# Kernel optimization log

Measured on AMD Instinct MI355X. Metric: run time of the kernel, lower is better.

## Reference

```python
import jax, jax.numpy as jnp
import numpy as np

D = 256; NH = 8; HD = D // NH; L = 4; P = 4; NQ = 900; BS = 8; DFFN = 1024
SHAPES = np.array([[128, 128], [64, 64], [32, 32], [16, 16]])  # (H, W) per level, static metadata
NV = int((SHAPES[:, 0] * SHAPES[:, 1]).sum())
EPS = 1e-6


def setup_inputs():
    key = jax.random.key(0)
    ks = iter(jax.random.split(key, 48))

    def nrm(shape, scale=0.02):
        return jax.random.normal(next(ks), shape, jnp.float32) * scale

    lsi = np.concatenate([[0], np.cumsum(SHAPES[:, 0] * SHAPES[:, 1])[:-1]]).astype(np.int64)
    return {
        'tgt': nrm((NQ, BS, D), 1.0),
        'tgt_query_pos': nrm((NQ, BS, D), 1.0),
        'tgt_reference_points': jax.random.uniform(next(ks), (NQ, BS, L, 2), jnp.float32),
        'memory': nrm((NV, BS, D), 1.0),
        'memory_spatial_shapes': jnp.asarray(SHAPES, jnp.int32),
        'memory_level_start_index': jnp.asarray(lsi, jnp.int32),
        'w_norm_sa': jnp.ones((D,), jnp.float32),
        'w_norm_ca': jnp.ones((D,), jnp.float32),
        'w_norm_ffn': jnp.ones((D,), jnp.float32),
        'ls_sa': jnp.full((D,), 1e-4, jnp.float32),
        'ls_ca': jnp.full((D,), 1e-4, jnp.float32),
        'ls_ffn': jnp.full((D,), 1e-4, jnp.float32),
        'Wq': nrm((D, D)), 'Wk': nrm((D, D)), 'Wv': nrm((D, D)),
        'bq': jnp.zeros((D,), jnp.float32), 'bk': jnp.zeros((D,), jnp.float32), 'bv': jnp.zeros((D,), jnp.float32),
        'Wo_sa': nrm((D, D)), 'bo_sa': jnp.zeros((D,), jnp.float32),
        'Wv_proj': nrm((D, D)), 'bv_proj': jnp.zeros((D,), jnp.float32),
        'W_off': nrm((NH * L * P * 2, D)), 'b_off': nrm((NH * L * P * 2,), 0.1),
        'W_attn': nrm((NH * L * P, D)), 'b_attn': jnp.zeros((NH * L * P,), jnp.float32),
        'W_out_ca': nrm((D, D)), 'bo_ca': jnp.zeros((D,), jnp.float32),
        'Wg': nrm((DFFN, D)), 'bg': jnp.zeros((DFFN,), jnp.float32),
        'Wu': nrm((DFFN, D)), 'bu': jnp.zeros((DFFN,), jnp.float32),
        'Wf': nrm((D, DFFN)), 'bf': jnp.zeros((D,), jnp.float32),
    }


def rmsnorm(x, w):
    return x * jax.lax.rsqrt(jnp.mean(x * x, axis=-1, keepdims=True) + EPS) * w


def ms_deform_sample(v, loc, attw):
    # v: (bs, nv, NH, HD); loc: (bs, nq, NH, L, P, 2) normalized (x, y); attw: (bs, nq, NH, L, P)
    bs, nq = loc.shape[0], loc.shape[1]
    out = jnp.zeros((bs, nq, NH, HD), loc.dtype)
    b_idx = jnp.arange(bs)[:, None, None, None]
    h_idx = jnp.arange(NH)[None, None, :, None]
    start = 0
    for l in range(L):
        Hl, Wl = int(SHAPES[l, 0]), int(SHAPES[l, 1])
        vf = v[:, start:start + Hl * Wl]  # (bs, Hl*Wl, NH, HD)
        start += Hl * Wl
        # grid_sample(align_corners=False, padding=zeros) pixel mapping
        x = loc[:, :, :, l, :, 0] * Wl - 0.5
        y = loc[:, :, :, l, :, 1] * Hl - 0.5
        x0 = jnp.floor(x)
        y0 = jnp.floor(y)
        acc = jnp.zeros((bs, nq, NH, P, HD), loc.dtype)
        for dx in (0, 1):
            for dy in (0, 1):
                xi = x0 + dx
                yi = y0 + dy
                w = (1.0 - jnp.abs(x - xi)) * (1.0 - jnp.abs(y - yi))
                valid = (xi >= 0) & (xi <= Wl - 1) & (yi >= 0) & (yi <= Hl - 1)
                w = jnp.where(valid, w, 0.0)
                idx = (jnp.clip(yi, 0, Hl - 1) * Wl + jnp.clip(xi, 0, Wl - 1)).astype(jnp.int32)
                acc = acc + w[..., None] * vf[b_idx, idx, h_idx]  # (bs, nq, NH, P, HD)
        out = out + jnp.einsum('bqhp,bqhpd->bqhd', attw[:, :, :, l], acc)
    return out


def reference(tgt, tgt_query_pos, tgt_reference_points, memory, memory_spatial_shapes,
              memory_level_start_index, w_norm_sa, w_norm_ca, w_norm_ffn, ls_sa, ls_ca, ls_ffn,
              Wq, Wk, Wv, bq, bk, bv, Wo_sa, bo_sa, Wv_proj, bv_proj, W_off, b_off, W_attn,
              b_attn, W_out_ca, bo_ca, Wg, bg, Wu, bu, Wf, bf):
    nq, bs, d = tgt.shape
    # --- self-attention (pre-norm + LayerScale residual) ---
    xn = rmsnorm(tgt, w_norm_sa)
    qk = xn + tgt_query_pos
    q = (qk @ Wq.T + bq).reshape(nq, bs, NH, HD)
    k = (qk @ Wk.T + bk).reshape(nq, bs, NH, HD)
    vv = (xn @ Wv.T + bv).reshape(nq, bs, NH, HD)
    scores = jnp.einsum('qbhd,kbhd->bhqk', q, k) * (1.0 / np.sqrt(HD))
    attn = jax.nn.softmax(scores, axis=-1)
    sa = jnp.einsum('bhqk,kbhd->qbhd', attn, vv).reshape(nq, bs, d) @ Wo_sa.T + bo_sa
    tgt = tgt + ls_sa * sa
    # --- multi-scale deformable cross-attention (identity=zeros in original) ---
    xn = rmsnorm(tgt, w_norm_ca)
    qca = jnp.swapaxes(xn + tgt_query_pos, 0, 1)  # (bs, nq, d)
    val = (jnp.swapaxes(memory, 0, 1) @ Wv_proj.T + bv_proj).reshape(bs, -1, NH, HD)
    off = (qca @ W_off.T + b_off).reshape(bs, nq, NH, L, P, 2)
    attw = jax.nn.softmax((qca @ W_attn.T + b_attn).reshape(bs, nq, NH, L * P), axis=-1)
    attw = attw.reshape(bs, nq, NH, L, P)
    norm = jnp.asarray(SHAPES[:, ::-1].copy(), jnp.float32)  # (W, H) per level
    ref = jnp.swapaxes(tgt_reference_points, 0, 1)  # (bs, nq, L, 2)
    loc = ref[:, :, None, :, None, :] + off / norm[None, None, None, :, None, :]
    ca = ms_deform_sample(val, loc, attw).reshape(bs, nq, d) @ W_out_ca.T + bo_ca
    tgt = tgt + ls_ca * jnp.swapaxes(ca, 0, 1)
    # --- SwiGLU FFN ---
    xn = rmsnorm(tgt, w_norm_ffn)
    ffn = (jax.nn.silu(xn @ Wg.T + bg) * (xn @ Wu.T + bu)) @ Wf.T + bf
    return tgt + ls_ffn * ffn
```

## Files before the change

kernel.cpp:

```cpp
#include <hip/hip_runtime.h>

typedef unsigned short ushort_t;
typedef unsigned int uint32;
typedef __bf16 bf16x8 __attribute__((ext_vector_type(8)));
typedef float f32x4 __attribute__((ext_vector_type(4)));
typedef ushort_t us4 __attribute__((ext_vector_type(4)));

#define D_    256
#define NH_   8
#define HD_   32
#define NQ_   900
#define BS_   8
#define TOK_  7200
#define NV_   21760
#define QP_   928
#define DFFN_ 1024

__device__ __forceinline__ ushort_t f2bf(float x) {
    union { float f; uint32 u; } v; v.f = x;
    uint32 r = v.u + 0x7FFFu + ((v.u >> 16) & 1u);
    return (ushort_t)(r >> 16);
}
__device__ __forceinline__ float bf2f(ushort_t h) {
    union { uint32 u; float f; } v; v.u = ((uint32)h) << 16;
    return v.f;
}
__device__ __forceinline__ int imin(int a, int b) { return a < b ? a : b; }
__device__ __forceinline__ int imax(int a, int b) { return a > b ? a : b; }

__global__ __launch_bounds__(256) void cvtall_k(
    const float* __restrict__ s0, const float* __restrict__ s1, const float* __restrict__ s2,
    const float* __restrict__ s3, const float* __restrict__ s4, const float* __restrict__ s5,
    const float* __restrict__ s6, const float* __restrict__ s7, const float* __restrict__ s8,
    const float* __restrict__ s9, const float* __restrict__ s10, ushort_t* __restrict__ dst,
    const float* __restrict__ bq, const float* __restrict__ bk, const float* __restrict__ bv,
    const float* __restrict__ boff, const float* __restrict__ battn,
    float* __restrict__ bias_qkv, float* __restrict__ bias_ol) {
    int tid = threadIdx.x;
    if (blockIdx.x == 0) {
        bias_qkv[tid] = bq[tid];
        bias_qkv[256 + tid] = bk[tid];
        bias_qkv[512 + tid] = bv[tid];
        bias_ol[tid] = boff[tid];
        if (tid < 128) bias_ol[256 + tid] = battn[tid];
    }
    int id = blockIdx.x * 256 + tid;
    const float* s; int off;
    if      (id <  16384) { s = s0;  off = id; }
    else if (id <  32768) { s = s1;  off = id - 16384; }
    else if (id <  49152) { s = s2;  off = id - 32768; }
    else if (id <  65536) { s = s3;  off = id - 49152; }
    else if (id <  81920) { s = s4;  off = id - 65536; }
    else if (id <  98304) { s = s5;  off = id - 81920; }
    else if (id < 114688) { s = s6;  off = id - 98304; }
    else if (id < 122880) { s = s7;  off = id - 114688; }
    else if (id < 188416) { s = s8;  off = id - 122880; }
    else if (id < 253952) { s = s9;  off = id - 188416; }
    else                  { s = s10; off = id - 253952; }
    f32x4 v = *(const f32x4*)(s + (size_t)off * 4);
    us4 t;
#pragma unroll
    for (int e = 0; e < 4; e++) t[e] = f2bf(v[e]);
    *(us4*)(dst + (size_t)id * 4) = t;
}

__global__ __launch_bounds__(256) void rms_k(const float* __restrict__ x,
                                             const float* __restrict__ pos,
                                             const float* __restrict__ wn,
                                             ushort_t* __restrict__ xn_out,
                                             ushort_t* __restrict__ qk_out) {
    const int r = blockIdx.x * 4 + (threadIdx.x >> 6);
    const int lane = threadIdx.x & 63;
    const size_t base = (size_t)r * D_ + lane * 4;
    f32x4 v = *(const f32x4*)(x + base);
    float ss = v[0] * v[0] + v[1] * v[1] + v[2] * v[2] + v[3] * v[3];
#pragma unroll
    for (int o = 32; o; o >>= 1) ss += __shfl_xor(ss, o, 64);
    float sc = rsqrtf(ss * (1.f / 256.f) + 1e-6f);
    f32x4 wv = *(const f32x4*)(wn + lane * 4);
    if (xn_out) {
        us4 t;
#pragma unroll
        for (int e = 0; e < 4; e++) t[e] = f2bf(v[e] * sc * wv[e]);
        *(us4*)(xn_out + base) = t;
    }
    if (qk_out) {
        f32x4 p = *(const f32x4*)(pos + base);
        us4 t;
#pragma unroll
        for (int e = 0; e < 4; e++) t[e] = f2bf(v[e] * sc * wv[e] + p[e]);
        *(us4*)(qk_out + base) = t;
    }
}

enum { EPI_RESID, EPI_QKV, EPI_OFFLOG };

template <int EPI, bool AF32, int BM, int BN, int WGM, int WGN, int TK>
__global__ __launch_bounds__(WGM * WGN * 64) void gemm2_k(
    const void* __restrict__ Ap, const void* __restrict__ Ap2,
    const ushort_t* __restrict__ Wp,
    const float* __restrict__ bias, void* __restrict__ outp, void* __restrict__ outp2,
    void* __restrict__ outp3, int M, int N, int swz,
    const float* __restrict__ resid, const float* __restrict__ ls, float scale) {
    constexpr int THREADS = WGM * WGN * 64;
    constexpr int NK  = TK / 32;
    constexpr int LDK = 40;
    constexpr int WR  = BM / WGM, WC = BN / WGN;
    constexpr int FM  = WR / 16,  FN = WC / 16;
    constexpr int ACH = AF32 ? (BM * 32 / 4 / THREADS) : (BM * 32 / 8 / THREADS);
    constexpr int BCH = BN * 32 / 8 / THREADS;

    __shared__ __align__(16) ushort_t As[2][BM * LDK];
    __shared__ __align__(16) ushort_t Bs[2][BN * LDK];

    const int tid = threadIdx.x, l = tid & 63, w = tid >> 6;
    const int wm = w % WGM, wn = w / WGM;
    int by = blockIdx.y;
    if (swz) { int cpx = gridDim.y >> 3; by = (by & 7) * cpx + (by >> 3); }
    const int m0 = by * BM, n0 = blockIdx.x * BN;
    const int lr = l & 15, lkb = (l >> 4) * 8;

    const void* Asel = (EPI == EPI_QKV && n0 >= 512) ? Ap2 : Ap;
    const ushort_t* Ab = (const ushort_t*)Asel;
    const float*    Af = (const float*)Asel;

    int aRow[ACH], aK[ACH], bRow[BCH], bK[BCH];
#pragma unroll
    for (int ch = 0; ch < ACH; ch++) {
        int cid = ch * THREADS + tid;
        if constexpr (AF32) { aRow[ch] = cid >> 3; aK[ch] = (cid & 7) * 4; }
        else                { aRow[ch] = cid >> 2; aK[ch] = (cid & 3) * 8; }
    }
#pragma unroll
    for (int ch = 0; ch < BCH; ch++) {
        int cid = ch * THREADS + tid;
        bRow[ch] = cid >> 2; bK[ch] = (cid & 3) * 8;
    }
    int aGRow[ACH];
#pragma unroll
    for (int ch = 0; ch < ACH; ch++) aGRow[ch] = imin(m0 + aRow[ch], M - 1);

    f32x4  aSTf[AF32 ? ACH : 1];
    bf16x8 aSTb[AF32 ? 1 : ACH];
    bf16x8 bST[BCH];

    auto load_regs = [&](int kt) {
        const int k0 = kt * 32;
#pragma unroll
        for (int ch = 0; ch < ACH; ch++) {
            if constexpr (AF32)
                aSTf[ch] = *(const f32x4*)(Af + (size_t)aGRow[ch] * TK + k0 + aK[ch]);
            else
                aSTb[ch] = *(const bf16x8*)(Ab + (size_t)aGRow[ch] * TK + k0 + aK[ch]);
        }
#pragma unroll
        for (int ch = 0; ch < BCH; ch++)
            bST[ch] = *(const bf16x8*)(Wp + (size_t)(n0 + bRow[ch]) * TK + k0 + bK[ch]);
    };
    auto write_lds = [&](int buf) {
#pragma unroll
        for (int ch = 0; ch < ACH; ch++) {
            if constexpr (AF32) {
                us4 t;
#pragma unroll
                for (int e = 0; e < 4; e++) t[e] = f2bf(aSTf[ch][e]);
                *(us4*)&As[buf][aRow[ch] * LDK + aK[ch]] = t;
            } else {
                *(bf16x8*)&As[buf][aRow[ch] * LDK + aK[ch]] = aSTb[ch];
            }
        }
#pragma unroll
        for (int ch = 0; ch < BCH; ch++)
            *(bf16x8*)&Bs[buf][bRow[ch] * LDK + bK[ch]] = bST[ch];
    };

    f32x4 acc[FM][FN];
#pragma unroll
    for (int i = 0; i < FM; i++)
#pragma unroll
        for (int j = 0; j < FN; j++) acc[i][j] = f32x4{0.f, 0.f, 0.f, 0.f};

    load_regs(0);
    write_lds(0);
    __syncthreads();

    for (int kt = 0; kt < NK; ++kt) {
        const int c = kt & 1;
        if (kt + 1 < NK) load_regs(kt + 1);

        bf16x8 af[FM], bf_[FN];
#pragma unroll
        for (int i = 0; i < FM; i++)
            af[i] = *(const bf16x8*)&As[c][(wm * WR + i * 16 + lr) * LDK + lkb];
#pragma unroll
        for (int j = 0; j < FN; j++)
            bf_[j] = *(const bf16x8*)&Bs[c][(wn * WC + j * 16 + lr) * LDK + lkb];
#pragma unroll
        for (int i = 0; i < FM; i++)
#pragma unroll
            for (int j = 0; j < FN; j++)
                acc[i][j] = __builtin_amdgcn_mfma_f32_16x16x32_bf16(af[i], bf_[j], acc[i][j], 0, 0, 0);

        if (kt + 1 < NK) write_lds(c ^ 1);
        __syncthreads();
    }

#pragma unroll
    for (int i = 0; i < FM; i++)
#pragma unroll
        for (int j = 0; j < FN; j++) {
            int col = n0 + wn * WC + j * 16 + lr;
            float bvv = bias[col];
#pragma unroll
            for (int e = 0; e < 4; e++) {
                int row = m0 + wm * WR + i * 16 + (l >> 4) * 4 + e;
                if (row >= M) continue;
                float v = acc[i][j][e] + bvv;
                if constexpr (EPI == EPI_RESID) {
                    size_t idx = (size_t)row * N + col;
                    ((float*)outp)[idx] = resid[idx] + ls[col] * v;
                } else if constexpr (EPI == EPI_QKV) {
                    int c2 = col & 255;
                    int q = row >> 3, bb = row & 7, h = c2 >> 5, hd = c2 & 31;
                    if (col < 256) {
                        ((ushort_t*)outp)[((bb * NH_ + h) * QP_ + q) * HD_ + hd] = f2bf(v * scale);
                    } else if (col < 512) {
                        ((ushort_t*)outp2)[((bb * NH_ + h) * QP_ + q) * HD_ + hd] = f2bf(v);
                    } else {
                        ((ushort_t*)outp3)[((bb * NH_ + h) * HD_ + hd) * QP_ + q] = f2bf(v);
                    }
                } else if constexpr (EPI == EPI_OFFLOG) {
                    if (col < 256) ((float*)outp)[(size_t)row * 256 + col] = v;
                    else           ((float*)outp2)[(size_t)row * 128 + col - 256] = v;
                }
            }
        }
}

__global__ __launch_bounds__(512) void gemm4_k(
    const float* __restrict__ Af, const ushort_t* __restrict__ Wp,
    const float* __restrict__ bias, ushort_t* __restrict__ outp, int swz) {
    constexpr int TK = 256, NK = 4, LDK = 72;
    __shared__ __align__(16) ushort_t As[2][64 * LDK];

    const int tid = threadIdx.x, l = tid & 63, w = tid >> 6;
    int by = blockIdx.y;
    if (swz) { int cpx = gridDim.y >> 3; by = (by & 7) * cpx + (by >> 3); }
    const int m0 = by * 64;
    const int lr = l & 15, g = l >> 4, lkb = g * 8;

    const int aRow = tid >> 3, aK = (tid & 7) * 4;
    const float* aPtr = Af + (size_t)(m0 + aRow) * TK + aK;
    f32x4 aST0, aST1;
    auto loadA = [&](int kt) {
        aST0 = *(const f32x4*)(aPtr + kt * 64);
        aST1 = *(const f32x4*)(aPtr + kt * 64 + 32);
    };
    auto writeA = [&](int buf) {
        us4 t0, t1;
#pragma unroll
        for (int e = 0; e < 4; e++) { t0[e] = f2bf(aST0[e]); t1[e] = f2bf(aST1[e]); }
        *(us4*)&As[buf][aRow * LDK + aK] = t0;
        *(us4*)&As[buf][aRow * LDK + 32 + aK] = t1;
    };

    const ushort_t* bPtr0 = Wp + (size_t)(w * 32 + lr) * TK + lkb;
    const ushort_t* bPtr1 = Wp + (size_t)(w * 32 + 16 + lr) * TK + lkb;

    f32x4 acc[4][2];
#pragma unroll
    for (int i = 0; i < 4; i++)
#pragma unroll
        for (int j = 0; j < 2; j++) acc[i][j] = f32x4{0.f, 0.f, 0.f, 0.f};

    bf16x8 bC[2][2], bN[2][2];
    loadA(0);
#pragma unroll
    for (int kk = 0; kk < 2; kk++) {
        bC[kk][0] = *(const bf16x8*)(bPtr0 + kk * 32);
        bC[kk][1] = *(const bf16x8*)(bPtr1 + kk * 32);
    }
    writeA(0);
    __syncthreads();

    for (int kt = 0; kt < NK; ++kt) {
        const int c = kt & 1;
        if (kt + 1 < NK) {
            loadA(kt + 1);
#pragma unroll
            for (int kk = 0; kk < 2; kk++) {
                bN[kk][0] = *(const bf16x8*)(bPtr0 + (kt + 1) * 64 + kk * 32);
                bN[kk][1] = *(const bf16x8*)(bPtr1 + (kt + 1) * 64 + kk * 32);
            }
        }
#pragma unroll
        for (int kk = 0; kk < 2; kk++) {
            bf16x8 af[4];
#pragma unroll
            for (int i = 0; i < 4; i++)
                af[i] = *(const bf16x8*)&As[c][(i * 16 + lr) * LDK + kk * 32 + lkb];
#pragma unroll
            for (int i = 0; i < 4; i++) {
                acc[i][0] = __builtin_amdgcn_mfma_f32_16x16x32_bf16(af[i], bC[kk][0], acc[i][0], 0, 0, 0);
                acc[i][1] = __builtin_amdgcn_mfma_f32_16x16x32_bf16(af[i], bC[kk][1], acc[i][1], 0, 0, 0);
            }
        }
        if (kt + 1 < NK) writeA(c ^ 1);
        __syncthreads();
#pragma unroll
        for (int kk = 0; kk < 2; kk++) {
            bC[kk][0] = bN[kk][0];
            bC[kk][1] = bN[kk][1];
        }
    }

#pragma unroll
    for (int i = 0; i < 4; i++)
#pragma unroll
        for (int j = 0; j < 2; j++) {
            int col = w * 32 + j * 16 + lr;
            float bvv = bias[col];
            int h = col >> 5, d = col & 31;
#pragma unroll
            for (int e = 0; e < 4; e++) {
                int row = m0 + i * 16 + g * 4 + e;
                int vv = row >> 3, bb = row & 7;
                outp[(((size_t)(bb * NH_ + h)) * NV_ + vv) * HD_ + d] = f2bf(acc[i][j][e] + bvv);
            }
        }
}

__global__ __launch_bounds__(256) void ffn_k(
    const ushort_t* __restrict__ Ap, const ushort_t* __restrict__ Wg,
    const ushort_t* __restrict__ Wu, const float* __restrict__ bgp,
    const float* __restrict__ bup, ushort_t* __restrict__ outp, int M) {
    constexpr int BM = 64, BN = 128, TK = 256, NK = TK / 32, LDK = 40;
    constexpr int WR = 32, WC = 64, FM = 2, FN = 4;

    __shared__ __align__(16) ushort_t As[2][BM * LDK];
    __shared__ __align__(16) ushort_t Gs[2][BN * LDK];
    __shared__ __align__(16) ushort_t Us[2][BN * LDK];

    const int tid = threadIdx.x, l = tid & 63, w = tid >> 6;
    const int wm = w & 1, wn = w >> 1;
    const int m0 = blockIdx.y * BM, n0 = blockIdx.x * BN;
    const int lr = l & 15, lkb = (l >> 4) * 8;

    const int aRow = tid >> 2, aK = (tid & 3) * 8;
    int bRow[2], bK[2];
#pragma unroll
    for (int ch = 0; ch < 2; ch++) { int cid = ch * 256 + tid; bRow[ch] = cid >> 2; bK[ch] = (cid & 3) * 8; }
    const int aGRow = imin(m0 + aRow, M - 1);

    bf16x8 aST, gST[2], uST[2];
    auto load_regs = [&](int kt) {
        const int k0 = kt * 32;
        aST = *(const bf16x8*)(Ap + (size_t)aGRow * TK + k0 + aK);
#pragma unroll
        for (int ch = 0; ch < 2; ch++) {
            gST[ch] = *(const bf16x8*)(Wg + (size_t)(n0 + bRow[ch]) * TK + k0 + bK[ch]);
            uST[ch] = *(const bf16x8*)(Wu + (size_t)(n0 + bRow[ch]) * TK + k0 + bK[ch]);
        }
    };
    auto write_lds = [&](int buf) {
        *(bf16x8*)&As[buf][aRow * LDK + aK] = aST;
#pragma unroll
        for (int ch = 0; ch < 2; ch++) {
            *(bf16x8*)&Gs[buf][bRow[ch] * LDK + bK[ch]] = gST[ch];
            *(bf16x8*)&Us[buf][bRow[ch] * LDK + bK[ch]] = uST[ch];
        }
    };

    f32x4 accG[FM][FN], accU[FM][FN];
#pragma unroll
    for (int i = 0; i < FM; i++)
#pragma unroll
        for (int j = 0; j < FN; j++) { accG[i][j] = f32x4{0,0,0,0}; accU[i][j] = f32x4{0,0,0,0}; }

    load_regs(0);
    write_lds(0);
    __syncthreads();

    for (int kt = 0; kt < NK; ++kt) {
        const int c = kt & 1;
        if (kt + 1 < NK) load_regs(kt + 1);
        bf16x8 af[FM], gf[FN], uf[FN];
#pragma unroll
        for (int i = 0; i < FM; i++)
            af[i] = *(const bf16x8*)&As[c][(wm * WR + i * 16 + lr) * LDK + lkb];
#pragma unroll
        for (int j = 0; j < FN; j++) {
            gf[j] = *(const bf16x8*)&Gs[c][(wn * WC + j * 16 + lr) * LDK + lkb];
            uf[j] = *(const bf16x8*)&Us[c][(wn * WC + j * 16 + lr) * LDK + lkb];
        }
#pragma unroll
        for (int i = 0; i < FM; i++)
#pragma unroll
            for (int j = 0; j < FN; j++) {
                accG[i][j] = __builtin_amdgcn_mfma_f32_16x16x32_bf16(af[i], gf[j], accG[i][j], 0, 0, 0);
                accU[i][j] = __builtin_amdgcn_mfma_f32_16x16x32_bf16(af[i], uf[j], accU[i][j], 0, 0, 0);
            }
        if (kt + 1 < NK) write_lds(c ^ 1);
        __syncthreads();
    }

#pragma unroll
    for (int i = 0; i < FM; i++)
#pragma unroll
        for (int j = 0; j < FN; j++) {
            int col = n0 + wn * WC + j * 16 + lr;
            float bg_ = bgp[col], bu_ = bup[col];
#pragma unroll
            for (int e = 0; e < 4; e++) {
                int row = m0 + wm * WR + i * 16 + (l >> 4) * 4 + e;
                if (row >= M) continue;
                float g = accG[i][j][e] + bg_;
                float u = accU[i][j][e] + bu_;
                float s = g / (1.f + __expf(-g));
                outp[(size_t)row * DFFN_ + col] = f2bf(s * u);
            }
        }
}

__global__ __launch_bounds__(256) void attn2_k(const ushort_t* __restrict__ qb,
                                               const ushort_t* __restrict__ kb,
                                               const ushort_t* __restrict__ vtb,
                                               ushort_t* __restrict__ sab) {
    __shared__ __align__(16) ushort_t Pl[4][16 * 40];
    const int tid = threadIdx.x, l = tid & 63, w = tid >> 6;
    const int bh = blockIdx.y, b = bh >> 3, h = bh & 7;
    const int q0 = (blockIdx.x * 4 + w) * 16;
    if (q0 >= NQ_) return;
    const int q = l & 15, g = l >> 4;
    ushort_t* Pw = &Pl[w][0];

    const bf16x8 qf = *(const bf16x8*)(qb + ((size_t)bh * QP_ + q0 + q) * HD_ + g * 8);
    const ushort_t* kbase = kb + (size_t)bh * QP_ * HD_;
    const ushort_t* vbase = vtb + (size_t)bh * HD_ * QP_;

    f32x4 O0 = {0.f, 0.f, 0.f, 0.f}, O1 = {0.f, 0.f, 0.f, 0.f};
    float m = -1e30f, sl = 0.f;

    auto ldk = [&](int t, int u) {
        return *(const bf16x8*)(kbase + (size_t)(t * 32 + u * 16 + q) * HD_ + g * 8);
    };
    auto ldv = [&](int t, int dh) {
        return *(const bf16x8*)(vbase + (size_t)(dh * 16 + q) * QP_ + t * 32 + g * 8);
    };
    bf16x8 kA = ldk(0, 0), kB = ldk(0, 1), v0 = ldv(0, 0), v1 = ldv(0, 1);

    for (int t = 0; t < 29; ++t) {
        bf16x8 nkA, nkB, nv0, nv1;
        if (t < 28) { nkA = ldk(t + 1, 0); nkB = ldk(t + 1, 1); nv0 = ldv(t + 1, 0); nv1 = ldv(t + 1, 1); }
        const f32x4 z = {0.f, 0.f, 0.f, 0.f};
        f32x4 sA = __builtin_amdgcn_mfma_f32_16x16x32_bf16(kA, qf, z, 0, 0, 0);
        f32x4 sB = __builtin_amdgcn_mfma_f32_16x16x32_bf16(kB, qf, z, 0, 0, 0);
        if (t == 28) {
            int k0 = 896 + g * 4;
#pragma unroll
            for (int e = 0; e < 4; e++) {
                if (k0 + e >= NQ_)      sA[e] = -1e30f;
                if (k0 + 16 + e >= NQ_) sB[e] = -1e30f;
            }
        }
        float tm = fmaxf(fmaxf(fmaxf(sA[0], sA[1]), fmaxf(sA[2], sA[3])),
                         fmaxf(fmaxf(sB[0], sB[1]), fmaxf(sB[2], sB[3])));
        tm = fmaxf(tm, __shfl_xor(tm, 16, 64));
        tm = fmaxf(tm, __shfl_xor(tm, 32, 64));
        float mn = fmaxf(m, tm);
        float r = exp2f(m - mn);
        m = mn;
#pragma unroll
        for (int e = 0; e < 4; e++) { O0[e] *= r; O1[e] *= r; }
        float pA[4], pB[4], ps = 0.f;
#pragma unroll
        for (int e = 0; e < 4; e++) {
            pA[e] = exp2f(sA[e] - m); pB[e] = exp2f(sB[e] - m);
            ps += pA[e] + pB[e];
        }
        sl = sl * r + ps;
        uint32 a0, a1, b0, b1;
        asm("v_cvt_pk_bf16_f32 %0, %1, %2" : "=v"(a0) : "v"(pA[0]), "v"(pA[1]));
        asm("v_cvt_pk_bf16_f32 %0, %1, %2" : "=v"(a1) : "v"(pA[2]), "v"(pA[3]));
        asm("v_cvt_pk_bf16_f32 %0, %1, %2" : "=v"(b0) : "v"(pB[0]), "v"(pB[1]));
        asm("v_cvt_pk_bf16_f32 %0, %1, %2" : "=v"(b1) : "v"(pB[2]), "v"(pB[3]));
        { uint2 tt; tt.x = a0; tt.y = a1; *(uint2*)(Pw + q * 40 + g * 4) = tt; }
        { uint2 tt; tt.x = b0; tt.y = b1; *(uint2*)(Pw + q * 40 + 16 + g * 4) = tt; }
        bf16x8 pf = *(const bf16x8*)(Pw + q * 40 + g * 8);
        O0 = __builtin_amdgcn_mfma_f32_16x16x32_bf16(v0, pf, O0, 0, 0, 0);
        O1 = __builtin_amdgcn_mfma_f32_16x16x32_bf16(v1, pf, O1, 0, 0, 0);
        kA = nkA; kB = nkB; v0 = nv0; v1 = nv1;
    }

    sl += __shfl_xor(sl, 16, 64);
    sl += __shfl_xor(sl, 32, 64);
    float inv = 1.f / sl;
    int row_q = q0 + q;
    if (row_q < NQ_) {
        ushort_t* op = sab + ((size_t)row_q * BS_ + b) * D_ + h * HD_ + g * 4;
#pragma unroll
        for (int dh = 0; dh < 2; dh++) {
            f32x4 Ov = dh ? O1 : O0;
            float e0 = Ov[0] * inv, e1 = Ov[1] * inv, e2 = Ov[2] * inv, e3 = Ov[3] * inv;
            uint32 w0, w1;
            asm("v_cvt_pk_bf16_f32 %0, %1, %2" : "=v"(w0) : "v"(e0), "v"(e1));
            asm("v_cvt_pk_bf16_f32 %0, %1, %2" : "=v"(w1) : "v"(e2), "v"(e3));
            *(uint32*)(op + dh * 16) = w0;
            *(uint32*)(op + dh * 16 + 2) = w1;
        }
    }
}

__global__ __launch_bounds__(256) void deform_k(
    const float* __restrict__ offb, const float* __restrict__ logb,
    const float* __restrict__ refpts, const int* __restrict__ shapes,
    const int* __restrict__ lsi, const ushort_t* __restrict__ val,
    ushort_t* __restrict__ ca) {
    __shared__ float off_l[256];
    __shared__ float attw[128];
    const int r = blockIdx.x;
    const int b = r & 7;
    const int tid = threadIdx.x;

    off_l[tid] = offb[(size_t)r * 256 + tid];
    if (tid < 128) {
        float lg = logb[(size_t)r * 128 + tid];
        float m = lg;
#pragma unroll
        for (int o = 1; o < 16; o <<= 1) m = fmaxf(m, __shfl_xor(m, o, 16));
        float e = __expf(lg - m);
        float s = e;
#pragma unroll
        for (int o = 1; o < 16; o <<= 1) s += __shfl_xor(s, o, 16);
        attw[tid] = e / s;
    }
    __syncthreads();

    const int h = tid >> 5, d = tid & 31;
    const ushort_t* vb = val + ((size_t)(b * NH_ + h)) * NV_ * HD_;
    float acc = 0.f;
#pragma unroll
    for (int lvl = 0; lvl < 4; lvl++) {
        const int H = shapes[lvl * 2], W = shapes[lvl * 2 + 1];
        const int base = lsi[lvl];
        const float refx = refpts[(r * 4 + lvl) * 2];
        const float refy = refpts[(r * 4 + lvl) * 2 + 1];
#pragma unroll
        for (int p = 0; p < 4; p++) {
            int oi = ((h * 4 + lvl) * 4 + p) * 2;
            float x = (refx + off_l[oi] / (float)W) * (float)W - 0.5f;
            float y = (refy + off_l[oi + 1] / (float)H) * (float)H - 0.5f;
            float x0 = floorf(x), y0 = floorf(y);
            float fx = x - x0, fy = y - y0;
            int ix = (int)x0, iy = (int)y0;
            float sval = 0.f;
#pragma unroll
            for (int dy = 0; dy <= 1; dy++)
#pragma unroll
                for (int dx = 0; dx <= 1; dx++) {
                    int xi = ix + dx, yi = iy + dy;
                    float wq = (dx ? fx : 1.f - fx) * (dy ? fy : 1.f - fy);
                    if (xi < 0 || xi >= W || yi < 0 || yi >= H) wq = 0.f;
                    int cx = imin(imax(xi, 0), W - 1), cy = imin(imax(yi, 0), H - 1);
                    float vv = bf2f(vb[(size_t)(base + cy * W + cx) * HD_ + d]);
                    sval += wq * vv;
                }
            acc += attw[h * 16 + lvl * 4 + p] * sval;
        }
    }
    ca[(size_t)r * 256 + tid] = f2bf(acc);
}

extern "C" void kernel_launch(void* const* d_in, const int* in_sizes, int n_in,
                              void* d_out, int out_size, void* d_ws, size_t ws_size,
                              hipStream_t stream) {
    (void)in_sizes; (void)n_in; (void)out_size; (void)ws_size;
    const float* tgt    = (const float*)d_in[0];
    const float* qpos   = (const float*)d_in[1];
    const float* refp   = (const float*)d_in[2];
    const float* mem    = (const float*)d_in[3];
    const int*   shapes = (const int*)d_in[4];
    const int*   lsi    = (const int*)d_in[5];
    const float* wnsa   = (const float*)d_in[6];
    const float* wnca   = (const float*)d_in[7];
    const float* wnffn  = (const float*)d_in[8];
    const float* lssa   = (const float*)d_in[9];
    const float* lsca   = (const float*)d_in[10];
    const float* lsffn  = (const float*)d_in[11];
    const float* Wq = (const float*)d_in[12];
    const float* Wk = (const float*)d_in[13];
    const float* Wv = (const float*)d_in[14];
    const float* bq = (const float*)d_in[15];
    const float* bk = (const float*)d_in[16];
    const float* bvv = (const float*)d_in[17];
    const float* Wo_sa = (const float*)d_in[18];
    const float* bo_sa = (const float*)d_in[19];
    const float* Wv_proj = (const float*)d_in[20];
    const float* bv_proj = (const float*)d_in[21];
    const float* W_off = (const float*)d_in[22];
    const float* b_off = (const float*)d_in[23];
    const float* W_attn = (const float*)d_in[24];
    const float* b_attn = (const float*)d_in[25];
    const float* W_out = (const float*)d_in[26];
    const float* bo_ca = (const float*)d_in[27];
    const float* Wg = (const float*)d_in[28];
    const float* bg = (const float*)d_in[29];
    const float* Wu = (const float*)d_in[30];
    const float* bu = (const float*)d_in[31];
    const float* Wf = (const float*)d_in[32];
    const float* bff = (const float*)d_in[33];

    char* ws = (char*)d_ws;
    size_t o = 0;
    auto alloc = [&](size_t b) { size_t c = o; o += (b + 255) & ~(size_t)255; return c; };

    const size_t wq_o = alloc(65536 * 2), wk_o = alloc(65536 * 2), wv_o = alloc(65536 * 2);
    const size_t wosa_o = alloc(65536 * 2), wvp_o = alloc(65536 * 2), wout_o = alloc(65536 * 2);
    const size_t woff_o = alloc(65536 * 2), wattn_o = alloc(32768 * 2);
    const size_t wg_o = alloc(262144 * 2), wu_o = alloc(262144 * 2), wf_o = alloc(262144 * 2);
    const size_t bqkv_o = alloc(768 * 4), bol_o = alloc(384 * 4);
    const size_t xnsa_o = alloc((size_t)TOK_ * D_ * 2);
    const size_t qksa_o = alloc((size_t)TOK_ * D_ * 2);
    const size_t qkvBytes = (size_t)BS_ * NH_ * QP_ * HD_ * 2;
    const size_t qb_o = alloc(qkvBytes);
    const size_t kb_o = alloc(qkvBytes);
    const size_t vt_o = alloc(qkvBytes + 512);
    const size_t sa_o = alloc((size_t)TOK_ * D_ * 2);
    const size_t tgt1_o = alloc((size_t)TOK_ * D_ * 4);
    const size_t qca_o = alloc((size_t)TOK_ * D_ * 2);
    const size_t offb_o = alloc((size_t)TOK_ * 256 * 4);
    const size_t logit_o = alloc((size_t)TOK_ * 128 * 4);
    const size_t ca_o = alloc((size_t)TOK_ * D_ * 2);
    const size_t tgt2_o = alloc((size_t)TOK_ * D_ * 4);
    const size_t val_o = alloc((size_t)NV_ * BS_ * D_ * 2);
    const size_t h_o  = val_o;
    const size_t xn3_o = h_o + (size_t)TOK_ * DFFN_ * 2;

    dim3 blk(256);
    cvtall_k<<<dim3(319488 / 256), blk, 0, stream>>>(
        Wq, Wk, Wv, Wo_sa, Wv_proj, W_out, W_off, W_attn, Wg, Wu, Wf,
        (ushort_t*)(ws + wq_o),
        bq, bk, bvv, b_off, b_attn, (float*)(ws + bqkv_o), (float*)(ws + bol_o));


    rms_k<<<dim3(TOK_ / 4), blk, 0, stream>>>(tgt, qpos, wnsa,
                                              (ushort_t*)(ws + xnsa_o), (ushort_t*)(ws + qksa_o));
    const float QSC = 0.25503321550239915f;
    gemm2_k<EPI_QKV, false, 64, 128, 2, 2, 256><<<dim3(6, 113), blk, 0, stream>>>(
        ws + qksa_o, ws + xnsa_o, (ushort_t*)(ws + wq_o), (const float*)(ws + bqkv_o),
        ws + qb_o, ws + kb_o, ws + vt_o, TOK_, 768, 0, nullptr, nullptr, QSC);
    attn2_k<<<dim3(15, 64), blk, 0, stream>>>((ushort_t*)(ws + qb_o), (ushort_t*)(ws + kb_o),
                                              (ushort_t*)(ws + vt_o), (ushort_t*)(ws + sa_o));
    gemm2_k<EPI_RESID, false, 64, 128, 2, 2, 256><<<dim3(2, 113), blk, 0, stream>>>(
        ws + sa_o, nullptr, (ushort_t*)(ws + wosa_o), bo_sa, ws + tgt1_o, nullptr, nullptr,
        TOK_, 256, 0, tgt, lssa, 1.f);

    rms_k<<<dim3(TOK_ / 4), blk, 0, stream>>>((const float*)(ws + tgt1_o), qpos, wnca,
                                              nullptr, (ushort_t*)(ws + qca_o));
    gemm2_k<EPI_OFFLOG, false, 64, 128, 2, 2, 256><<<dim3(3, 113), blk, 0, stream>>>(
        ws + qca_o, nullptr, (ushort_t*)(ws + woff_o), (const float*)(ws + bol_o),
        ws + offb_o, ws + logit_o, nullptr, TOK_, 384, 0, nullptr, nullptr, 1.f);
    gemm4_k<<<dim3(1, 2720), dim3(512), 0, stream>>>(
        mem, (ushort_t*)(ws + wvp_o), bv_proj, (ushort_t*)(ws + val_o), 1);
    deform_k<<<dim3(TOK_), blk, 0, stream>>>(
        (const float*)(ws + offb_o), (const float*)(ws + logit_o), refp, shapes, lsi,
        (ushort_t*)(ws + val_o), (ushort_t*)(ws + ca_o));
    gemm2_k<EPI_RESID, false, 64, 128, 2, 2, 256><<<dim3(2, 113), blk, 0, stream>>>(
        ws + ca_o, nullptr, (ushort_t*)(ws + wout_o), bo_ca, ws + tgt2_o, nullptr, nullptr,
        TOK_, 256, 0, (const float*)(ws + tgt1_o), lsca, 1.f);

    rms_k<<<dim3(TOK_ / 4), blk, 0, stream>>>((const float*)(ws + tgt2_o), nullptr, wnffn,
                                              (ushort_t*)(ws + xn3_o), nullptr);
    ffn_k<<<dim3(8, 113), blk, 0, stream>>>(
        (const ushort_t*)(ws + xn3_o), (const ushort_t*)(ws + wg_o),
        (const ushort_t*)(ws + wu_o), bg, bu, (ushort_t*)(ws + h_o), TOK_);
    gemm2_k<EPI_RESID, false, 64, 128, 2, 2, 1024><<<dim3(2, 113), blk, 0, stream>>>(
        ws + h_o, nullptr, (ushort_t*)(ws + wf_o), bff, d_out, nullptr, nullptr,
        TOK_, 256, 0, (const float*)(ws + tgt2_o), lsffn, 1.f);
}
```

Baseline: 321.3 us.

## Load FFN weight fragments directly into registers, stage only activations in LDS

Rewrites the SwiGLU gate/up kernel and the down-projection GEMM. Each warp now owns a 32-column slice of the weights and loads its MFMA B-fragments straight from global memory into registers, prefetching the next K step. Only the activation tile passes through double-buffered LDS, using 64-wide K steps. This cuts LDS traffic and the number of barriers, at the cost of uncoalesced per-lane weight loads and more registers per thread.

```diff
diff --git a/kernel.cpp b/kernel.cpp
--- a/kernel.cpp
+++ b/kernel.cpp
@@ -330,94 +330,192 @@
         }
 }
 
-__global__ __launch_bounds__(256) void ffn_k(
+__global__ __launch_bounds__(256) void ffn2_k(
     const ushort_t* __restrict__ Ap, const ushort_t* __restrict__ Wg,
     const ushort_t* __restrict__ Wu, const float* __restrict__ bgp,
     const float* __restrict__ bup, ushort_t* __restrict__ outp, int M) {
-    constexpr int BM = 64, BN = 128, TK = 256, NK = TK / 32, LDK = 40;
-    constexpr int WR = 32, WC = 64, FM = 2, FN = 4;
-
-    __shared__ __align__(16) ushort_t As[2][BM * LDK];
-    __shared__ __align__(16) ushort_t Gs[2][BN * LDK];
-    __shared__ __align__(16) ushort_t Us[2][BN * LDK];
+    constexpr int TK = 256, NK = 4, LDK = 72;
+    __shared__ __align__(16) ushort_t As[2][64 * LDK];
 
     const int tid = threadIdx.x, l = tid & 63, w = tid >> 6;
-    const int wm = w & 1, wn = w >> 1;
-    const int m0 = blockIdx.y * BM, n0 = blockIdx.x * BN;
-    const int lr = l & 15, lkb = (l >> 4) * 8;
-
-    const int aRow = tid >> 2, aK = (tid & 3) * 8;
-    int bRow[2], bK[2];
-#pragma unroll
-    for (int ch = 0; ch < 2; ch++) { int cid = ch * 256 + tid; bRow[ch] = cid >> 2; bK[ch] = (cid & 3) * 8; }
+    const int m0 = blockIdx.y * 64, n0 = blockIdx.x * 128;
+    const int lr = l & 15, g = l >> 4, lkb = g * 8;
+
+    const int aRow = tid >> 2, aK = (tid & 3) * 16;
     const int aGRow = imin(m0 + aRow, M - 1);
-
-    bf16x8 aST, gST[2], uST[2];
-    auto load_regs = [&](int kt) {
-        const int k0 = kt * 32;
-        aST = *(const bf16x8*)(Ap + (size_t)aGRow * TK + k0 + aK);
-#pragma unroll
-        for (int ch = 0; ch < 2; ch++) {
-            gST[ch] = *(const bf16x8*)(Wg + (size_t)(n0 + bRow[ch]) * TK + k0 + bK[ch]);
-            uST[ch] = *(const bf16x8*)(Wu + (size_t)(n0 + bRow[ch]) * TK + k0 + bK[ch]);
-        }
-    };
-    auto write_lds = [&](int buf) {
-        *(bf16x8*)&As[buf][aRow * LDK + aK] = aST;
-#pragma unroll
-        for (int ch = 0; ch < 2; ch++) {
-            *(bf16x8*)&Gs[buf][bRow[ch] * LDK + bK[ch]] = gST[ch];
-            *(bf16x8*)&Us[buf][bRow[ch] * LDK + bK[ch]] = uST[ch];
-        }
-    };
-
-    f32x4 accG[FM][FN], accU[FM][FN];
-#pragma unroll
-    for (int i = 0; i < FM; i++)
-#pragma unroll
-        for (int j = 0; j < FN; j++) { accG[i][j] = f32x4{0,0,0,0}; accU[i][j] = f32x4{0,0,0,0}; }
-
-    load_regs(0);
-    write_lds(0);
+    const ushort_t* aPtr = Ap + (size_t)aGRow * TK + aK;
+    bf16x8 aST0, aST1;
+    auto loadA = [&](int kt) {
+        aST0 = *(const bf16x8*)(aPtr + kt * 64);
+        aST1 = *(const bf16x8*)(aPtr + kt * 64 + 8);
+    };
+    auto writeA = [&](int buf) {
+        *(bf16x8*)&As[buf][aRow * LDK + aK] = aST0;
+        *(bf16x8*)&As[buf][aRow * LDK + aK + 8] = aST1;
+    };
+
+    const ushort_t* gP0 = Wg + (size_t)(n0 + w * 32 + lr) * TK + lkb;
+    const ushort_t* gP1 = Wg + (size_t)(n0 + w * 32 + 16 + lr) * TK + lkb;
+    const ushort_t* uP0 = Wu + (size_t)(n0 + w * 32 + lr) * TK + lkb;
+    const ushort_t* uP1 = Wu + (size_t)(n0 + w * 32 + 16 + lr) * TK + lkb;
+
+    f32x4 accG[4][2], accU[4][2];
+#pragma unroll
+    for (int i = 0; i < 4; i++)
+#pragma unroll
+        for (int j = 0; j < 2; j++) { accG[i][j] = f32x4{0,0,0,0}; accU[i][j] = f32x4{0,0,0,0}; }
+
+    bf16x8 gC[2][2], uC[2][2], gN[2][2], uN[2][2];
+    loadA(0);
+#pragma unroll
+    for (int kk = 0; kk < 2; kk++) {
+        gC[kk][0] = *(const bf16x8*)(gP0 + kk * 32);
+        gC[kk][1] = *(const bf16x8*)(gP1 + kk * 32);
+        uC[kk][0] = *(const bf16x8*)(uP0 + kk * 32);
+        uC[kk][1] = *(const bf16x8*)(uP1 + kk * 32);
+    }
+    writeA(0);
     __syncthreads();
 
     for (int kt = 0; kt < NK; ++kt) {
         const int c = kt & 1;
-        if (kt + 1 < NK) load_regs(kt + 1);
-        bf16x8 af[FM], gf[FN], uf[FN];
-#pragma unroll
-        for (int i = 0; i < FM; i++)
-            af[i] = *(const bf16x8*)&As[c][(wm * WR + i * 16 + lr) * LDK + lkb];
-#pragma unroll
-        for (int j = 0; j < FN; j++) {
-            gf[j] = *(const bf16x8*)&Gs[c][(wn * WC + j * 16 + lr) * LDK + lkb];
-            uf[j] = *(const bf16x8*)&Us[c][(wn * WC + j * 16 + lr) * LDK + lkb];
-        }
-#pragma unroll
-        for (int i = 0; i < FM; i++)
-#pragma unroll
-            for (int j = 0; j < FN; j++) {
-                accG[i][j] = __builtin_amdgcn_mfma_f32_16x16x32_bf16(af[i], gf[j], accG[i][j], 0, 0, 0);
-                accU[i][j] = __builtin_amdgcn_mfma_f32_16x16x32_bf16(af[i], uf[j], accU[i][j], 0, 0, 0);
-            }
-        if (kt + 1 < NK) write_lds(c ^ 1);
+        if (kt + 1 < NK) {
+            loadA(kt + 1);
+#pragma unroll
+            for (int kk = 0; kk < 2; kk++) {
+                gN[kk][0] = *(const bf16x8*)(gP0 + (kt + 1) * 64 + kk * 32);
+                gN[kk][1] = *(const bf16x8*)(gP1 + (kt + 1) * 64 + kk * 32);
+                uN[kk][0] = *(const bf16x8*)(uP0 + (kt + 1) * 64 + kk * 32);
+                uN[kk][1] = *(const bf16x8*)(uP1 + (kt + 1) * 64 + kk * 32);
+            }
+        }
+#pragma unroll
+        for (int kk = 0; kk < 2; kk++) {
+            bf16x8 af[4];
+#pragma unroll
+            for (int i = 0; i < 4; i++)
+                af[i] = *(const bf16x8*)&As[c][(i * 16 + lr) * LDK + kk * 32 + lkb];
+#pragma unroll
+            for (int i = 0; i < 4; i++) {
+                accG[i][0] = __builtin_amdgcn_mfma_f32_16x16x32_bf16(af[i], gC[kk][0], accG[i][0], 0, 0, 0);
+                accG[i][1] = __builtin_amdgcn_mfma_f32_16x16x32_bf16(af[i], gC[kk][1], accG[i][1], 0, 0, 0);
+                accU[i][0] = __builtin_amdgcn_mfma_f32_16x16x32_bf16(af[i], uC[kk][0], accU[i][0], 0, 0, 0);
+                accU[i][1] = __builtin_amdgcn_mfma_f32_16x16x32_bf16(af[i], uC[kk][1], accU[i][1], 0, 0, 0);
+            }
+        }
+        if (kt + 1 < NK) writeA(c ^ 1);
         __syncthreads();
-    }
-
-#pragma unroll
-    for (int i = 0; i < FM; i++)
-#pragma unroll
-        for (int j = 0; j < FN; j++) {
-            int col = n0 + wn * WC + j * 16 + lr;
+#pragma unroll
+        for (int kk = 0; kk < 2; kk++) {
+            gC[kk][0] = gN[kk][0]; gC[kk][1] = gN[kk][1];
+            uC[kk][0] = uN[kk][0]; uC[kk][1] = uN[kk][1];
+        }
+    }
+
+#pragma unroll
+    for (int i = 0; i < 4; i++)
+#pragma unroll
+        for (int j = 0; j < 2; j++) {
+            int col = n0 + w * 32 + j * 16 + lr;
             float bg_ = bgp[col], bu_ = bup[col];
 #pragma unroll
             for (int e = 0; e < 4; e++) {
-                int row = m0 + wm * WR + i * 16 + (l >> 4) * 4 + e;
+                int row = m0 + i * 16 + g * 4 + e;
                 if (row >= M) continue;
-                float g = accG[i][j][e] + bg_;
-                float u = accU[i][j][e] + bu_;
-                float s = g / (1.f + __expf(-g));
-                outp[(size_t)row * DFFN_ + col] = f2bf(s * u);
+                float gg = accG[i][j][e] + bg_;
+                float uu = accU[i][j][e] + bu_;
+                float s = gg / (1.f + __expf(-gg));
+                outp[(size_t)row * DFFN_ + col] = f2bf(s * uu);
+            }
+        }
+}
+
+__global__ __launch_bounds__(256) void down_k(
+    const ushort_t* __restrict__ Ap, const ushort_t* __restrict__ Wf,
+    const float* __restrict__ bias, float* __restrict__ outp, int M,
+    const float* __restrict__ resid, const float* __restrict__ ls) {
+    constexpr int TK = 1024, NK = 16, LDK = 72;
+    __shared__ __align__(16) ushort_t As[2][64 * LDK];
+
+    const int tid = threadIdx.x, l = tid & 63, w = tid >> 6;
+    const int m0 = blockIdx.y * 64, n0 = blockIdx.x * 128;
+    const int lr = l & 15, g = l >> 4, lkb = g * 8;
+
+    const int aRow = tid >> 2, aK = (tid & 3) * 16;
+    const int aGRow = imin(m0 + aRow, M - 1);
+    const ushort_t* aPtr = Ap + (size_t)aGRow * TK + aK;
+    bf16x8 aST0, aST1;
+    auto loadA = [&](int kt) {
+        aST0 = *(const bf16x8*)(aPtr + kt * 64);
+        aST1 = *(const bf16x8*)(aPtr + kt * 64 + 8);
+    };
+    auto writeA = [&](int buf) {
+        *(bf16x8*)&As[buf][aRow * LDK + aK] = aST0;
+        *(bf16x8*)&As[buf][aRow * LDK + aK + 8] = aST1;
+    };
+
+    const ushort_t* bP0 = Wf + (size_t)(n0 + w * 32 + lr) * TK + lkb;
+    const ushort_t* bP1 = Wf + (size_t)(n0 + w * 32 + 16 + lr) * TK + lkb;
+
+    f32x4 acc[4][2];
+#pragma unroll
+    for (int i = 0; i < 4; i++)
+#pragma unroll
+        for (int j = 0; j < 2; j++) acc[i][j] = f32x4{0.f, 0.f, 0.f, 0.f};
+
+    bf16x8 bC[2][2], bN[2][2];
+    loadA(0);
+#pragma unroll
+    for (int kk = 0; kk < 2; kk++) {
+        bC[kk][0] = *(const bf16x8*)(bP0 + kk * 32);
+        bC[kk][1] = *(const bf16x8*)(bP1 + kk * 32);
+    }
+    writeA(0);
+    __syncthreads();
+
+    for (int kt = 0; kt < NK; ++kt) {
+        const int c = kt & 1;
+        if (kt + 1 < NK) {
+            loadA(kt + 1);
+#pragma unroll
+            for (int kk = 0; kk < 2; kk++) {
+                bN[kk][0] = *(const bf16x8*)(bP0 + (kt + 1) * 64 + kk * 32);
+                bN[kk][1] = *(const bf16x8*)(bP1 + (kt + 1) * 64 + kk * 32);
+            }
+        }
+#pragma unroll
+        for (int kk = 0; kk < 2; kk++) {
+            bf16x8 af[4];
+#pragma unroll
+            for (int i = 0; i < 4; i++)
+                af[i] = *(const bf16x8*)&As[c][(i * 16 + lr) * LDK + kk * 32 + lkb];
+#pragma unroll
+            for (int i = 0; i < 4; i++) {
+                acc[i][0] = __builtin_amdgcn_mfma_f32_16x16x32_bf16(af[i], bC[kk][0], acc[i][0], 0, 0, 0);
+                acc[i][1] = __builtin_amdgcn_mfma_f32_16x16x32_bf16(af[i], bC[kk][1], acc[i][1], 0, 0, 0);
+            }
+        }
+        if (kt + 1 < NK) writeA(c ^ 1);
+        __syncthreads();
+#pragma unroll
+        for (int kk = 0; kk < 2; kk++) {
+            bC[kk][0] = bN[kk][0];
+            bC[kk][1] = bN[kk][1];
+        }
+    }
+
+#pragma unroll
+    for (int i = 0; i < 4; i++)
+#pragma unroll
+        for (int j = 0; j < 2; j++) {
+            int col = n0 + w * 32 + j * 16 + lr;
+            float bvv = bias[col], lsc = ls[col];
+#pragma unroll
+            for (int e = 0; e < 4; e++) {
+                int row = m0 + i * 16 + g * 4 + e;
+                if (row >= M) continue;
+                size_t idx = (size_t)row * 256 + col;
+                outp[idx] = resid[idx] + lsc * (acc[i][j][e] + bvv);
             }
         }
 }
@@ -671,10 +769,10 @@
 
     rms_k<<<dim3(TOK_ / 4), blk, 0, stream>>>((const float*)(ws + tgt2_o), nullptr, wnffn,
                                               (ushort_t*)(ws + xn3_o), nullptr);
-    ffn_k<<<dim3(8, 113), blk, 0, stream>>>(
+    ffn2_k<<<dim3(8, 113), blk, 0, stream>>>(
         (const ushort_t*)(ws + xn3_o), (const ushort_t*)(ws + wg_o),
         (const ushort_t*)(ws + wu_o), bg, bu, (ushort_t*)(ws + h_o), TOK_);
-    gemm2_k<EPI_RESID, false, 64, 128, 2, 2, 1024><<<dim3(2, 113), blk, 0, stream>>>(
-        ws + h_o, nullptr, (ushort_t*)(ws + wf_o), bff, d_out, nullptr, nullptr,
-        TOK_, 256, 0, (const float*)(ws + tgt2_o), lsffn, 1.f);
-}
+    down_k<<<dim3(2, 113), blk, 0, stream>>>(
+        (const ushort_t*)(ws + h_o), (const ushort_t*)(ws + wf_o), bff,
+        (float*)d_out, TOK_, (const float*)(ws + tgt2_o), lsffn);
+}
```

Result: no change. 322.9 us (+0.5%).
